# Kernel optimization log

Hardware: AMD Instinct MI355X
Metric: run time of the kernel (lower is better)

Reference implementation:

```python
import jax, jax.numpy as jnp
import numpy as np

N = 4096
CIN = 128
COUT = 128
J = 2
SLOPE = 0.2        # LeakyReLU negative slope (GAT-style)
NEG = -9.0e15      # mask fill value from the source
ATT = J * COUT     # att_slice


def _leaky(v):
    return jnp.where(v >= 0, v, SLOPE * v)


def setup_inputs() -> dict:
    key = jax.random.key(0)
    ks = jax.random.split(key, 12)
    x = jax.random.normal(ks[0], (N, CIN), dtype=jnp.float32)

    def sparse_op(k):
        kv, km = jax.random.split(k)
        vals = jax.random.normal(kv, (N, N), dtype=jnp.float32)
        mask = jax.random.uniform(km, (N, N)) < 0.05
        return jnp.where(mask, vals, 0.0)

    Lu = sparse_op(ks[1])
    Ld = sparse_op(ks[2])
    P = jax.random.normal(ks[3], (N, N), dtype=jnp.float32) * 0.01  # harmonic projector

    s = 1.0 / np.sqrt(CIN)
    Wi_w = jax.random.uniform(ks[4], (J, CIN, COUT), minval=-s, maxval=s)
    Wi_b = jax.random.uniform(ks[5], (J, COUT), minval=-s, maxval=s)
    Ws_w = jax.random.uniform(ks[6], (J, CIN, COUT), minval=-s, maxval=s)
    Ws_b = jax.random.uniform(ks[7], (J, COUT), minval=-s, maxval=s)
    Wh_w = jax.random.uniform(ks[8], (CIN, COUT), minval=-s, maxval=s)
    Wh_b = jax.random.uniform(ks[9], (COUT,), minval=-s, maxval=s)
    att_irr = jax.random.normal(ks[10], (2 * ATT, 1), dtype=jnp.float32) * 0.1
    att_sol = jax.random.normal(ks[11], (2 * ATT, 1), dtype=jnp.float32) * 0.1
    return {"x": x, "Lu": Lu, "Ld": Ld, "P": P,
            "Wi_w": Wi_w, "Wi_b": Wi_b, "Ws_w": Ws_w, "Ws_b": Ws_b,
            "Wh_w": Wh_w, "Wh_b": Wh_b, "att_irr": att_irr, "att_sol": att_sol}


def reference(x, Lu, Ld, P, Wi_w, Wi_b, Ws_w, Ws_b, Wh_w, Wh_b, att_irr, att_sol):
    n = x.shape[0]
    # concat_j W_irr[j](x) -> [N, J*COUT] (j-major matches torch.cat along dim=1)
    x_irr = (jnp.einsum('nc,jco->njo', x, Wi_w) + Wi_b[None]).reshape(n, ATT)
    x_sol = (jnp.einsum('nc,jco->njo', x, Ws_w) + Ws_b[None]).reshape(n, ATT)

    # GAT-style scores: E[i,j] = leaky(s1[i] + s2[j])
    E_irr = _leaky(x_irr @ att_irr[:ATT] + (x_irr @ att_irr[ATT:]).T)
    E_sol = _leaky(x_sol @ att_sol[:ATT] + (x_sol @ att_sol[ATT:]).T)
    E_irr = jnp.where(Ld != 0, E_irr, NEG)
    E_sol = jnp.where(Lu != 0, E_sol, NEG)
    alpha_irr = jax.nn.softmax(E_irr, axis=1)  # dropout: eval mode -> identity
    alpha_sol = jax.nn.softmax(E_sol, axis=1)

    z = (alpha_irr @ x) @ Wi_w[0] + Wi_b[0] + (alpha_sol @ x) @ Ws_w[0] + Ws_b[0]
    for p in range(1, J):  # Laplacian-power aggregation
        alpha_irr = alpha_irr @ Ld
        alpha_sol = alpha_sol @ Lu
        z = z + (alpha_irr @ x) @ Wi_w[p] + Wi_b[p]
        z = z + (alpha_sol @ x) @ Ws_w[p] + Ws_b[p]
    z = z + (P @ x) @ Wh_w + Wh_b
    return z
```

## Files before the change

kernel.cpp:

```cpp
#include <hip/hip_runtime.h>

#define NN 4096
#define SLOPE 0.2f

typedef float f4_t __attribute__((ext_vector_type(4)));
typedef __bf16 bf8v __attribute__((ext_vector_type(8)));
typedef float f32x16 __attribute__((ext_vector_type(16)));

#define V_OFF     0
#define C_OFF     512
#define BT_OFF    516
#define S_OFF     1024
#define HXI_OFF   32768
#define HXS_OFF   (HXI_OFF + NN*128)
#define UI_OFF    (HXS_OFF + NN*128)
#define US_OFF    (UI_OFF + NN*128)
#define XWH_OFF   (US_OFF + NN*128)
#define OI_OFF    (XWH_OFF + NN*128)
#define OS_OFF    (OI_OFF + NN*128)
#define ZP_OFF    (OS_OFF + NN*128)
#define WS_FLOATS (ZP_OFF + 8*NN*128)
#define XF_BYTE_OFF  ((size_t)WS_FLOATS * 4)
#define HX2_BYTE_OFF (XF_BYTE_OFF + (size_t)2*1024*1024)
#define DEN_BYTE_OFF (HX2_BYTE_OFF + (size_t)4*1024*1024)

#define XI(c)   ((c) + (((c) >> 5) << 2))

#define FRAG(c, k) ((size_t)((k) >> 4) * 2048 + (size_t)((c) >> 5) * 512 \
                    + (size_t)((((c) & 31) + 32 * (((k) >> 3) & 1)) * 8 + ((k) & 7)))

__device__ __forceinline__ unsigned short f2bf(float x) {
  unsigned u = __float_as_uint(x);
  return (unsigned short)((u + 0x7FFFu + ((u >> 16) & 1u)) >> 16);
}
__device__ __forceinline__ float bf2f(unsigned short h) {
  return __uint_as_float(((unsigned)h) << 16);
}
union BFU { unsigned short u[8]; bf8v v; };

__global__ __launch_bounds__(128) void k_prep(
    const float* __restrict__ Wi_w, const float* __restrict__ Wi_b,
    const float* __restrict__ Ws_w, const float* __restrict__ Ws_b,
    const float* __restrict__ Wh_b, const float* __restrict__ att_irr,
    const float* __restrict__ att_sol, float* __restrict__ ws) {
  const int t = threadIdx.x;
  float v1i = 0.f, v2i = 0.f, v1s = 0.f, v2s = 0.f;
  for (int j = 0; j < 2; ++j) {
    for (int o = 0; o < 128; ++o) {
      const float wi = Wi_w[j*16384 + t*128 + o];
      const float wv = Ws_w[j*16384 + t*128 + o];
      v1i += wi * att_irr[j*128 + o];
      v2i += wi * att_irr[256 + j*128 + o];
      v1s += wv * att_sol[j*128 + o];
      v2s += wv * att_sol[256 + j*128 + o];
    }
  }
  ws[V_OFF + t]       = v1i;
  ws[V_OFF + 128 + t] = v2i;
  ws[V_OFF + 256 + t] = v1s;
  ws[V_OFF + 384 + t] = v2s;
  ws[BT_OFF + t] = Wi_b[t] + Wi_b[128 + t] + Ws_b[t] + Ws_b[128 + t] + Wh_b[t];
  if (t < 4) {
    const float* bb = (t < 2) ? Wi_b : Ws_b;
    const float* aa = ((t < 2) ? att_irr : att_sol) + ((t & 1) ? 256 : 0);
    float c = 0.f;
    for (int k = 0; k < 256; ++k) c += bb[k] * aa[k];
    ws[C_OFF + t] = c;
  }
}

__global__ __launch_bounds__(256) void k_pre2(
    const float* __restrict__ x, const float* __restrict__ Wh_w,
    float* __restrict__ ws, unsigned short* __restrict__ xth,
    unsigned short* __restrict__ xtl, unsigned short* __restrict__ xfh,
    unsigned short* __restrict__ xfl) {
  __shared__ __align__(16) float At[32][33];
  __shared__ __align__(16) float Wt[32][144];
  const int t = threadIdx.x;

  if (blockIdx.x < 128) {
    const int rb = blockIdx.x;
    const int rg = t >> 4, cg = t & 15;
    const int r0 = rb * 32;
    float acc[2][8];
    #pragma unroll
    for (int i = 0; i < 2; ++i)
      #pragma unroll
      for (int j = 0; j < 8; ++j) acc[i][j] = 0.f;
    for (int k0 = 0; k0 < 128; k0 += 32) {
      __syncthreads();
      {
        const int row = t >> 3, kq = t & 7;
        const float4 av = *(const float4*)&x[(r0 + row)*128 + k0 + kq*4];
        At[row][kq*4+0] = av.x; At[row][kq*4+1] = av.y;
        At[row][kq*4+2] = av.z; At[row][kq*4+3] = av.w;
      }
      #pragma unroll
      for (int l = 0; l < 4; ++l) {
        const int idx = t + l*256;
        const int kr = idx >> 5, c4 = idx & 31;
        const float4 wv = *(const float4*)&Wh_w[(k0 + kr)*128 + c4*4];
        *(float4*)&Wt[kr][XI(c4*4)] = wv;
      }
      __syncthreads();
      #pragma unroll
      for (int k = 0; k < 32; ++k) {
        const float a0 = At[rg*2 + 0][k];
        const float a1 = At[rg*2 + 1][k];
        const float4 b0 = *(const float4*)&Wt[k][XI(cg*8)];
        const float4 b1 = *(const float4*)&Wt[k][XI(cg*8 + 4)];
        acc[0][0] += a0*b0.x; acc[0][1] += a0*b0.y; acc[0][2] += a0*b0.z; acc[0][3] += a0*b0.w;
        acc[0][4] += a0*b1.x; acc[0][5] += a0*b1.y; acc[0][6] += a0*b1.z; acc[0][7] += a0*b1.w;
        acc[1][0] += a1*b0.x; acc[1][1] += a1*b0.y; acc[1][2] += a1*b0.z; acc[1][3] += a1*b0.w;
        acc[1][4] += a1*b1.x; acc[1][5] += a1*b1.y; acc[1][6] += a1*b1.z; acc[1][7] += a1*b1.w;
      }
    }
    #pragma unroll
    for (int i = 0; i < 2; ++i) {
      const int r = r0 + rg*2 + i;
      #pragma unroll
      for (int j = 0; j < 8; ++j) {
        const int c = cg*8 + j;
        const float val = acc[i][j];
        const unsigned short h = f2bf(val);
        const unsigned short l = f2bf(val - bf2f(h));
        const size_t fa = FRAG(c, r);
        xth[fa] = h;
        xtl[fa] = l;
      }
    }
  } else {
    const int wave = t >> 6, lane = t & 63;
    const int row = (blockIdx.x - 128) * 4 + wave;
    const float* v = ws + V_OFF;
    const float x0 = x[row*128 + lane];
    const float x1 = x[row*128 + 64 + lane];
    {
      const unsigned short h0 = f2bf(x0);
      const unsigned short l0 = f2bf(x0 - bf2f(h0));
      const size_t fa0 = FRAG(lane, row);
      xfh[fa0] = h0; xfl[fa0] = l0;
      const unsigned short h1 = f2bf(x1);
      const unsigned short l1 = f2bf(x1 - bf2f(h1));
      const size_t fa1 = FRAG(lane + 64, row);
      xfh[fa1] = h1; xfl[fa1] = l1;
    }
    float p0 = x0 * v[lane]       + x1 * v[64 + lane];
    float p1 = x0 * v[128 + lane] + x1 * v[192 + lane];
    float p2 = x0 * v[256 + lane] + x1 * v[320 + lane];
    float p3 = x0 * v[384 + lane] + x1 * v[448 + lane];
    #pragma unroll
    for (int off = 32; off; off >>= 1) {
      p0 += __shfl_down(p0, off);
      p1 += __shfl_down(p1, off);
      p2 += __shfl_down(p2, off);
      p3 += __shfl_down(p3, off);
    }
    if (lane == 0) {
      ws[S_OFF + row]          = p0 + ws[C_OFF + 0];
      ws[S_OFF + NN + row]     = p1 + ws[C_OFF + 1];
      ws[S_OFF + 2*NN + row]   = p2 + ws[C_OFF + 2];
      ws[S_OFF + 3*NN + row]   = p3 + ws[C_OFF + 3];
    }
  }
}

__global__ __launch_bounds__(512) void k_hxmm(
    const float* __restrict__ Ld, const float* __restrict__ Lu,
    const unsigned short* __restrict__ xfh, const unsigned short* __restrict__ xfl,
    float* __restrict__ ws, float* __restrict__ hx2) {
  const int bid = blockIdx.x;
  const int br  = (bid >> 2) & 1;
  const int rest = ((bid >> 3) << 2) | (bid & 3);
  const int rblk = rest & 127;
  const int kz   = rest >> 7;
  const int t = threadIdx.x;
  const int lane = t & 63;
  const int n = (t >> 6) & 3, par = t >> 8;
  const int r0 = rblk * 32;
  const int kbase = kz * 2048;
  const float* __restrict__ L = br ? Lu : Ld;
  float* __restrict__ out = kz ? (hx2 + (size_t)br * NN * 128)
                               : (ws + (br ? HXS_OFF : HXI_OFF));

  __shared__ __align__(16) char ahb[2][8192];
  __shared__ __align__(16) char alb[2][8192];

  f32x16 acc;
  #pragma unroll
  for (int e = 0; e < 16; ++e) acc[e] = 0.f;

  const int srow = t >> 4;
  const int kg   = (t & 15) * 8;
  const int sS   = kg >> 4;
  const int lt   = srow + 32 * ((kg >> 3) & 1);
  const int soff = (sS * 64 + (lt ^ sS)) * 16;
  const float* __restrict__ lrow = L + (size_t)(r0 + srow) * NN + kbase + kg;

  const unsigned short* __restrict__ bh_w =
      xfh + ((size_t)(kbase >> 4) + par * 4) * 2048 + n * 512 + lane * 8;
  const unsigned short* __restrict__ bl_w =
      xfl + ((size_t)(kbase >> 4) + par * 4) * 2048 + n * 512 + lane * 8;

  bf8v bhA[4], blA[4], bhB[4], blB[4];

  f4_t va = *(const f4_t*)lrow;
  f4_t vb = *(const f4_t*)(lrow + 4);
  #pragma unroll
  for (int si = 0; si < 4; ++si) {
    bhA[si] = *(const bf8v*)(bh_w + (size_t)si * 2048);
    blA[si] = *(const bf8v*)(bl_w + (size_t)si * 2048);
  }
  {
    BFU ph, pl;
    #pragma unroll
    for (int c = 0; c < 8; ++c) {
      const float f = (c < 4) ? va[c] : vb[c - 4];
      const unsigned short hh = f2bf(f);
      ph.u[c] = hh;
      pl.u[c] = f2bf(f - bf2f(hh));
    }
    *(bf8v*)(ahb[0] + soff) = ph.v;
    *(bf8v*)(alb[0] + soff) = pl.v;
  }

  for (int m = 0; m < 8; ++m) {
    const int t1 = 2 * m + 1;
    f4_t na = *(const f4_t*)(lrow + t1 * 128);
    f4_t nb = *(const f4_t*)(lrow + t1 * 128 + 4);
    #pragma unroll
    for (int si = 0; si < 4; ++si) {
      bhB[si] = *(const bf8v*)(bh_w + ((size_t)t1 * 8 + si) * 2048);
      blB[si] = *(const bf8v*)(bl_w + ((size_t)t1 * 8 + si) * 2048);
    }
    __syncthreads();
    #pragma unroll
    for (int si = 0; si < 4; ++si) {
      const int s = par * 4 + si;
      const int ra16 = (s * 64 + (lane ^ s)) * 16;
      const bf8v ah = *(const bf8v*)(ahb[0] + ra16);
      const bf8v al = *(const bf8v*)(alb[0] + ra16);
      acc = __builtin_amdgcn_mfma_f32_32x32x16_bf16(ah, bhA[si], acc, 0, 0, 0);
      acc = __builtin_amdgcn_mfma_f32_32x32x16_bf16(al, bhA[si], acc, 0, 0, 0);
      acc = __builtin_amdgcn_mfma_f32_32x32x16_bf16(ah, blA[si], acc, 0, 0, 0);
    }
    {
      BFU ph, pl;
      #pragma unroll
      for (int c = 0; c < 8; ++c) {
        const float f = (c < 4) ? na[c] : nb[c - 4];
        const unsigned short hh = f2bf(f);
        ph.u[c] = hh;
        pl.u[c] = f2bf(f - bf2f(hh));
      }
      *(bf8v*)(ahb[1] + soff) = ph.v;
      *(bf8v*)(alb[1] + soff) = pl.v;
    }
    if (m < 7) {
      va = *(const f4_t*)(lrow + (t1 + 1) * 128);
      vb = *(const f4_t*)(lrow + (t1 + 1) * 128 + 4);
      #pragma unroll
      for (int si = 0; si < 4; ++si) {
        bhA[si] = *(const bf8v*)(bh_w + ((size_t)(t1 + 1) * 8 + si) * 2048);
        blA[si] = *(const bf8v*)(bl_w + ((size_t)(t1 + 1) * 8 + si) * 2048);
      }
    }
    __syncthreads();
    #pragma unroll
    for (int si = 0; si < 4; ++si) {
      const int s = par * 4 + si;
      const int ra16 = (s * 64 + (lane ^ s)) * 16;
      const bf8v ah = *(const bf8v*)(ahb[1] + ra16);
      const bf8v al = *(const bf8v*)(alb[1] + ra16);
      acc = __builtin_amdgcn_mfma_f32_32x32x16_bf16(ah, bhB[si], acc, 0, 0, 0);
      acc = __builtin_amdgcn_mfma_f32_32x32x16_bf16(al, bhB[si], acc, 0, 0, 0);
      acc = __builtin_amdgcn_mfma_f32_32x32x16_bf16(ah, blB[si], acc, 0, 0, 0);
    }
    if (m < 7) {
      BFU ph, pl;
      #pragma unroll
      for (int c = 0; c < 8; ++c) {
        const float f = (c < 4) ? va[c] : vb[c - 4];
        const unsigned short hh = f2bf(f);
        ph.u[c] = hh;
        pl.u[c] = f2bf(f - bf2f(hh));
      }
      *(bf8v*)(ahb[0] + soff) = ph.v;
      *(bf8v*)(alb[0] + soff) = pl.v;
    }
  }

  float* red = (float*)&ahb[0][0];
  __syncthreads();
  const int la = lane & 31;
  if (par == 1) {
    #pragma unroll
    for (int reg = 0; reg < 16; ++reg) {
      const int row = (reg & 3) + 8*(reg >> 2) + 4*(lane >> 5);
      red[n*1024 + row*32 + la] = acc[reg];
    }
  }
  __syncthreads();
  if (par == 0) {
    #pragma unroll
    for (int reg = 0; reg < 16; ++reg) {
      const int row = (reg & 3) + 8*(reg >> 2) + 4*(lane >> 5);
      out[(size_t)(r0 + row) * 128 + n*32 + la] = acc[reg] + red[n*1024 + row*32 + la];
    }
  }
}

__global__ __launch_bounds__(256) void k_ugemm(
    const float* __restrict__ x, const float* __restrict__ Wi_w,
    const float* __restrict__ Ws_w, float* __restrict__ ws,
    const float* __restrict__ hx2,
    unsigned short* __restrict__ uih, unsigned short* __restrict__ uil,
    unsigned short* __restrict__ ush, unsigned short* __restrict__ usl) {
  const int rb = blockIdx.x;
  const int sel = blockIdx.y;
  const float* A[2]; const float* A2[2]; const float* W[2];
  unsigned short* uh; unsigned short* ul;
  if (sel == 0) { A[0]=x; A2[0]=nullptr; W[0]=Wi_w;
                  A[1]=ws+HXI_OFF; A2[1]=hx2; W[1]=Wi_w+16384; uh=uih; ul=uil; }
  else          { A[0]=x; A2[0]=nullptr; W[0]=Ws_w;
                  A[1]=ws+HXS_OFF; A2[1]=hx2+(size_t)NN*128; W[1]=Ws_w+16384; uh=ush; ul=usl; }

  __shared__ __align__(16) float At[32][33];
  __shared__ __align__(16) float Wt[32][144];
  const int t = threadIdx.x;
  const int rg = t >> 4, cg = t & 15;
  const int r0 = rb * 32;
  float acc[2][8];
  #pragma unroll
  for (int i = 0; i < 2; ++i)
    #pragma unroll
    for (int j = 0; j < 8; ++j) acc[i][j] = 0.f;

  for (int ps = 0; ps < 2; ++ps) {
    const float* __restrict__ Ap = A[ps];
    const float* __restrict__ Ap2 = A2[ps];
    const float* __restrict__ Wp = W[ps];
    for (int k0 = 0; k0 < 128; k0 += 32) {
      __syncthreads();
      {
        const int row = t >> 3, kq = t & 7;
        float4 av = *(const float4*)&Ap[(r0 + row)*128 + k0 + kq*4];
        if (Ap2) {
          const float4 av2 = *(const float4*)&Ap2[(r0 + row)*128 + k0 + kq*4];
          av.x += av2.x; av.y += av2.y; av.z += av2.z; av.w += av2.w;
        }
        At[row][kq*4+0] = av.x; At[row][kq*4+1] = av.y;
        At[row][kq*4+2] = av.z; At[row][kq*4+3] = av.w;
      }
      #pragma unroll
      for (int l = 0; l < 4; ++l) {
        const int idx = t + l*256;
        const int kr = idx >> 5, c4 = idx & 31;
        const float4 wv = *(const float4*)&Wp[(k0 + kr)*128 + c4*4];
        *(float4*)&Wt[kr][XI(c4*4)] = wv;
      }
      __syncthreads();
      #pragma unroll
      for (int k = 0; k < 32; ++k) {
        const float a0 = At[rg*2 + 0][k];
        const float a1 = At[rg*2 + 1][k];
        const float4 b0 = *(const float4*)&Wt[k][XI(cg*8)];
        const float4 b1 = *(const float4*)&Wt[k][XI(cg*8 + 4)];
        acc[0][0] += a0*b0.x; acc[0][1] += a0*b0.y; acc[0][2] += a0*b0.z; acc[0][3] += a0*b0.w;
        acc[0][4] += a0*b1.x; acc[0][5] += a0*b1.y; acc[0][6] += a0*b1.z; acc[0][7] += a0*b1.w;
        acc[1][0] += a1*b0.x; acc[1][1] += a1*b0.y; acc[1][2] += a1*b0.z; acc[1][3] += a1*b0.w;
        acc[1][4] += a1*b1.x; acc[1][5] += a1*b1.y; acc[1][6] += a1*b1.z; acc[1][7] += a1*b1.w;
      }
    }
  }
  #pragma unroll
  for (int i = 0; i < 2; ++i) {
    const int r = r0 + rg*2 + i;
    #pragma unroll
    for (int j = 0; j < 8; ++j) {
      const int c = cg*8 + j;
      const float val = acc[i][j];
      const unsigned short h = f2bf(val);
      const unsigned short l = f2bf(val - bf2f(h));
      const size_t fa = FRAG(c, r);
      uh[fa] = h;
      ul[fa] = l;
    }
  }
}

__global__ __launch_bounds__(512) void k_attnmm(
    const float* __restrict__ Ld, const float* __restrict__ Lu,
    float* __restrict__ ws, const unsigned short* __restrict__ uih,
    const unsigned short* __restrict__ uil, const unsigned short* __restrict__ ush,
    const unsigned short* __restrict__ usl, float* __restrict__ denp) {
  const int bid = blockIdx.x;
  const int br  = (bid >> 2) & 1;
  const int rest = ((bid >> 3) << 2) | (bid & 3);
  const int rblk = rest & 127;
  const int kz   = rest >> 7;
  const int t = threadIdx.x;
  const int lane = t & 63;
  const int n = (t >> 6) & 3, par = t >> 8;
  const int r0 = rblk * 32;
  const int kbase = kz * 2048;
  const float* __restrict__ L = br ? Lu : Ld;
  const unsigned short* __restrict__ ufh = br ? ush : uih;
  const unsigned short* __restrict__ ufl = br ? usl : uil;
  float* __restrict__ out = kz ? (ws + (br ? HXS_OFF : HXI_OFF))
                               : (ws + (br ? OS_OFF : OI_OFF));
  float* __restrict__ dout = denp + (size_t)(kz * 2 + br) * NN;
  const float* __restrict__ s1b = ws + S_OFF + (br ? 2*NN : 0) + r0;
  const float* __restrict__ s2b = ws + S_OFF + (br ? 3*NN : NN) + kbase;

  __shared__ __align__(16) char ahb[2][8192];
  __shared__ __align__(16) char alb[2][8192];
  __shared__ float dend[32][16];

  f32x16 acc;
  #pragma unroll
  for (int e = 0; e < 16; ++e) acc[e] = 0.f;
  float dp = 0.f;

  const int srow = t >> 4;
  const int kg   = (t & 15) * 8;
  const int sS   = kg >> 4;
  const int lt   = srow + 32 * ((kg >> 3) & 1);
  const int soff = (sS * 64 + (lt ^ sS)) * 16;
  const float s1v = s1b[srow];
  const float* __restrict__ lrow = L + (size_t)(r0 + srow) * NN + kbase + kg;
  const float* __restrict__ s2r  = s2b + kg;

  const unsigned short* __restrict__ bh_w =
      ufh + ((size_t)(kbase >> 4) + par * 4) * 2048 + n * 512 + lane * 8;
  const unsigned short* __restrict__ bl_w =
      ufl + ((size_t)(kbase >> 4) + par * 4) * 2048 + n * 512 + lane * 8;

  bf8v bhA[4], blA[4], bhB[4], blB[4];

  f4_t va = *(const f4_t*)lrow;
  f4_t vb = *(const f4_t*)(lrow + 4);
  f4_t sa = *(const f4_t*)s2r;
  f4_t sb = *(const f4_t*)(s2r + 4);
  #pragma unroll
  for (int si = 0; si < 4; ++si) {
    bhA[si] = *(const bf8v*)(bh_w + (size_t)si * 2048);
    blA[si] = *(const bf8v*)(bl_w + (size_t)si * 2048);
  }
  {
    BFU ph, pl;
    #pragma unroll
    for (int c = 0; c < 8; ++c) {
      const float Lv = (c < 4) ? va[c] : vb[c - 4];
      const float s2 = (c < 4) ? sa[c] : sb[c - 4];
      const float sc = s1v + s2;
      const float scl = sc >= 0.f ? sc : SLOPE * sc;
      const float ex = (Lv != 0.f) ? __expf(scl) : 0.f;
      dp += ex;
      const unsigned short hh = f2bf(ex);
      ph.u[c] = hh;
      pl.u[c] = f2bf(ex - bf2f(hh));
    }
    *(bf8v*)(ahb[0] + soff) = ph.v;
    *(bf8v*)(alb[0] + soff) = pl.v;
  }

  for (int m = 0; m < 8; ++m) {
    const int t1 = 2 * m + 1;
    f4_t na = *(const f4_t*)(lrow + t1 * 128);
    f4_t nb = *(const f4_t*)(lrow + t1 * 128 + 4);
    f4_t nsa = *(const f4_t*)(s2r + t1 * 128);
    f4_t nsb = *(const f4_t*)(s2r + t1 * 128 + 4);
    #pragma unroll
    for (int si = 0; si < 4; ++si) {
      bhB[si] = *(const bf8v*)(bh_w + ((size_t)t1 * 8 + si) * 2048);
      blB[si] = *(const bf8v*)(bl_w + ((size_t)t1 * 8 + si) * 2048);
    }
    __syncthreads();
    #pragma unroll
    for (int si = 0; si < 4; ++si) {
      const int s = par * 4 + si;
      const int ra16 = (s * 64 + (lane ^ s)) * 16;
      const bf8v ah = *(const bf8v*)(ahb[0] + ra16);
      const bf8v al = *(const bf8v*)(alb[0] + ra16);
      acc = __builtin_amdgcn_mfma_f32_32x32x16_bf16(ah, bhA[si], acc, 0, 0, 0);
      acc = __builtin_amdgcn_mfma_f32_32x32x16_bf16(al, bhA[si], acc, 0, 0, 0);
      acc = __builtin_amdgcn_mfma_f32_32x32x16_bf16(ah, blA[si], acc, 0, 0, 0);
    }
    {
      BFU ph, pl;
      #pragma unroll
      for (int c = 0; c < 8; ++c) {
        const float Lv = (c < 4) ? na[c] : nb[c - 4];
        const float s2 = (c < 4) ? nsa[c] : nsb[c - 4];
        const float sc = s1v + s2;
        const float scl = sc >= 0.f ? sc : SLOPE * sc;
        const float ex = (Lv != 0.f) ? __expf(scl) : 0.f;
        dp += ex;
        const unsigned short hh = f2bf(ex);
        ph.u[c] = hh;
        pl.u[c] = f2bf(ex - bf2f(hh));
      }
      *(bf8v*)(ahb[1] + soff) = ph.v;
      *(bf8v*)(alb[1] + soff) = pl.v;
    }
    if (m < 7) {
      va = *(const f4_t*)(lrow + (t1 + 1) * 128);
      vb = *(const f4_t*)(lrow + (t1 + 1) * 128 + 4);
      sa = *(const f4_t*)(s2r + (t1 + 1) * 128);
      sb = *(const f4_t*)(s2r + (t1 + 1) * 128 + 4);
      #pragma unroll
      for (int si = 0; si < 4; ++si) {
        bhA[si] = *(const bf8v*)(bh_w + ((size_t)(t1 + 1) * 8 + si) * 2048);
        blA[si] = *(const bf8v*)(bl_w + ((size_t)(t1 + 1) * 8 + si) * 2048);
      }
    }
    __syncthreads();
    #pragma unroll
    for (int si = 0; si < 4; ++si) {
      const int s = par * 4 + si;
      const int ra16 = (s * 64 + (lane ^ s)) * 16;
      const bf8v ah = *(const bf8v*)(ahb[1] + ra16);
      const bf8v al = *(const bf8v*)(alb[1] + ra16);
      acc = __builtin_amdgcn_mfma_f32_32x32x16_bf16(ah, bhB[si], acc, 0, 0, 0);
      acc = __builtin_amdgcn_mfma_f32_32x32x16_bf16(al, bhB[si], acc, 0, 0, 0);
      acc = __builtin_amdgcn_mfma_f32_32x32x16_bf16(ah, blB[si], acc, 0, 0, 0);
    }
    if (m < 7) {
      BFU ph, pl;
      #pragma unroll
      for (int c = 0; c < 8; ++c) {
        const float Lv = (c < 4) ? va[c] : vb[c - 4];
        const float s2 = (c < 4) ? sa[c] : sb[c - 4];
        const float sc = s1v + s2;
        const float scl = sc >= 0.f ? sc : SLOPE * sc;
        const float ex = (Lv != 0.f) ? __expf(scl) : 0.f;
        dp += ex;
        const unsigned short hh = f2bf(ex);
        ph.u[c] = hh;
        pl.u[c] = f2bf(ex - bf2f(hh));
      }
      *(bf8v*)(ahb[0] + soff) = ph.v;
      *(bf8v*)(alb[0] + soff) = pl.v;
    }
  }

  dend[srow][t & 15] = dp;
  float* red = (float*)&ahb[0][0];
  __syncthreads();
  if (t < 32) {
    float d = 0.f;
    #pragma unroll
    for (int i = 0; i < 16; ++i) d += dend[t][i];
    dout[r0 + t] = d;
  }
  const int la = lane & 31;
  if (par == 1) {
    #pragma unroll
    for (int reg = 0; reg < 16; ++reg) {
      const int row = (reg & 3) + 8*(reg >> 2) + 4*(lane >> 5);
      red[n*1024 + row*32 + la] = acc[reg];
    }
  }
  __syncthreads();
  if (par == 0) {
    #pragma unroll
    for (int reg = 0; reg < 16; ++reg) {
      const int row = (reg & 3) + 8*(reg >> 2) + 4*(lane >> 5);
      out[(size_t)(r0 + row) * 128 + n*32 + la] = acc[reg] + red[n*1024 + row*32 + la];
    }
  }
}

__global__ __launch_bounds__(256) void k_pgemm(
    const float* __restrict__ P, const unsigned short* __restrict__ xth,
    const unsigned short* __restrict__ xtl, float* __restrict__ zpart) {
  const int t = threadIdx.x;
  const int w = t >> 6, lane = t & 63;
  const int la = lane & 31;
  const int koff = (lane >> 5) * 8;
  const int r0 = blockIdx.x * 32;
  const int kz = blockIdx.y;
  const int kb = kz * 512 + w * 128;

  f32x16 acc[4];
  #pragma unroll
  for (int n = 0; n < 4; ++n)
    #pragma unroll
    for (int e = 0; e < 16; ++e) acc[n][e] = 0.f;

  const float* __restrict__ arow = P + (size_t)(r0 + la) * NN + kb + koff;
  const unsigned short* __restrict__ bh_base = xth + (size_t)kb * 128 + lane * 8;
  const unsigned short* __restrict__ bl_base = xtl + (size_t)kb * 128 + lane * 8;

  f4_t a0 = __builtin_nontemporal_load((const f4_t*)arow);
  f4_t a1 = __builtin_nontemporal_load((const f4_t*)(arow + 4));
  for (int s = 0; s < 8; ++s) {
    f4_t na0 = a0, na1 = a1;
    if (s < 7) {
      na0 = __builtin_nontemporal_load((const f4_t*)(arow + (s + 1) * 16));
      na1 = __builtin_nontemporal_load((const f4_t*)(arow + (s + 1) * 16 + 4));
    }
    BFU ah, al;
    #pragma unroll
    for (int i = 0; i < 8; ++i) {
      const float f = (i < 4) ? a0[i] : a1[i - 4];
      const unsigned short h = f2bf(f);
      ah.u[i] = h;
      al.u[i] = f2bf(f - bf2f(h));
    }
    const unsigned short* __restrict__ bh_s = bh_base + s * 2048;
    const unsigned short* __restrict__ bl_s = bl_base + s * 2048;
    #pragma unroll
    for (int n = 0; n < 4; ++n) {
      const bf8v bh = *(const bf8v*)(bh_s + n * 512);
      const bf8v bl = *(const bf8v*)(bl_s + n * 512);
      acc[n] = __builtin_amdgcn_mfma_f32_32x32x16_bf16(ah.v, bh, acc[n], 0, 0, 0);
      acc[n] = __builtin_amdgcn_mfma_f32_32x32x16_bf16(al.v, bh, acc[n], 0, 0, 0);
      acc[n] = __builtin_amdgcn_mfma_f32_32x32x16_bf16(ah.v, bl, acc[n], 0, 0, 0);
    }
    a0 = na0; a1 = na1;
  }

  __shared__ float red[2][32][128];
  if (w < 2) {
    #pragma unroll
    for (int n = 0; n < 4; ++n)
      #pragma unroll
      for (int reg = 0; reg < 16; ++reg) {
        const int row = (reg & 3) + 8*(reg >> 2) + 4*(lane >> 5);
        red[w][row][32*n + la] = acc[n][reg];
      }
  }
  __syncthreads();
  if (w >= 2) {
    #pragma unroll
    for (int n = 0; n < 4; ++n)
      #pragma unroll
      for (int reg = 0; reg < 16; ++reg) {
        const int row = (reg & 3) + 8*(reg >> 2) + 4*(lane >> 5);
        red[w - 2][row][32*n + la] += acc[n][reg];
      }
  }
  __syncthreads();
  float* __restrict__ zp = zpart + (size_t)kz * NN * 128;
  #pragma unroll
  for (int i = 0; i < 8; ++i) {
    const int row = w * 8 + i;
    zp[(size_t)(r0 + row) * 128 + lane]      = red[0][row][lane]      + red[1][row][lane];
    zp[(size_t)(r0 + row) * 128 + 64 + lane] = red[0][row][64 + lane] + red[1][row][64 + lane];
  }
}

__global__ __launch_bounds__(256) void k_combine(const float* __restrict__ ws,
                                                 const float* __restrict__ denp,
                                                 float* __restrict__ z) {
  const int i = blockIdx.x * 256 + threadIdx.x;
  const int col = i & 127;
  const int row = i >> 7;
  const float di = denp[row] + denp[2*NN + row];
  const float ds = denp[NN + row] + denp[3*NN + row];
  const float oi = ws[OI_OFF + i] + ws[HXI_OFF + i];
  const float os = ws[OS_OFF + i] + ws[HXS_OFF + i];
  float acc = ws[BT_OFF + col] + oi / di + os / ds;
  #pragma unroll
  for (int kz = 0; kz < 8; ++kz) acc += ws[ZP_OFF + kz*NN*128 + i];
  z[i] = acc;
}

extern "C" void kernel_launch(void* const* d_in, const int* in_sizes, int n_in,
                              void* d_out, int out_size, void* d_ws, size_t ws_size,
                              hipStream_t stream) {
  const float* x       = (const float*)d_in[0];
  const float* Lu      = (const float*)d_in[1];
  const float* Ld      = (const float*)d_in[2];
  const float* P       = (const float*)d_in[3];
  const float* Wi_w    = (const float*)d_in[4];
  const float* Wi_b    = (const float*)d_in[5];
  const float* Ws_w    = (const float*)d_in[6];
  const float* Ws_b    = (const float*)d_in[7];
  const float* Wh_w    = (const float*)d_in[8];
  const float* Wh_b    = (const float*)d_in[9];
  const float* att_irr = (const float*)d_in[10];
  const float* att_sol = (const float*)d_in[11];
  float* z  = (float*)d_out;
  float* ws = (float*)d_ws;
  float*          zpart = ws + ZP_OFF;
  unsigned short* xth   = (unsigned short*)(ws + XWH_OFF);
  unsigned short* xtl   = xth + (size_t)128 * NN;
  unsigned short* uih   = (unsigned short*)(ws + UI_OFF);
  unsigned short* uil   = uih + (size_t)128 * NN;
  unsigned short* ush   = (unsigned short*)(ws + US_OFF);
  unsigned short* usl   = ush + (size_t)128 * NN;
  unsigned short* xfh   = (unsigned short*)((char*)d_ws + XF_BYTE_OFF);
  unsigned short* xfl   = xfh + (size_t)128 * NN;
  float*          hx2   = (float*)((char*)d_ws + HX2_BYTE_OFF);
  float*          denp  = (float*)((char*)d_ws + DEN_BYTE_OFF);

  k_prep<<<1, 128, 0, stream>>>(Wi_w, Wi_b, Ws_w, Ws_b, Wh_b, att_irr, att_sol, ws);
  k_pre2<<<1152, 256, 0, stream>>>(x, Wh_w, ws, xth, xtl, xfh, xfl);
  k_hxmm<<<512, 512, 0, stream>>>(Ld, Lu, xfh, xfl, ws, hx2);
  {
    dim3 g(128, 2);
    k_ugemm<<<g, 256, 0, stream>>>(x, Wi_w, Ws_w, ws, hx2, uih, uil, ush, usl);
  }
  k_attnmm<<<512, 512, 0, stream>>>(Ld, Lu, ws, uih, uil, ush, usl, denp);
  {
    dim3 g(128, 8);
    k_pgemm<<<g, 256, 0, stream>>>(P, xth, xtl, zpart);
  }
  k_combine<<<NN * 128 / 256, 256, 0, stream>>>(ws, denp, z);
}
```

Baseline: 360.9 us.

## Cache nonzero bitmask of Ld/Lu in hxmm and reuse in attention matmul

While streaming Ld/Lu in k_hxmm, each thread packs a nonzero bitmask byte for its 8 elements and writes it to workspace. k_attnmm then reads this bitmask (1 bit per element) instead of re-reading the full fp32 Ld/Lu matrices (2×64MB), cutting global memory traffic in the attention kernel. The mask buffer reuses the zpart region, which k_pgemm overwrites only after k_attnmm has run. The cost is extra byte-sized scattered stores in k_hxmm.

```diff
diff --git a/kernel.cpp b/kernel.cpp
--- a/kernel.cpp
+++ b/kernel.cpp
@@ -168,7 +168,8 @@
 __global__ __launch_bounds__(512) void k_hxmm(
     const float* __restrict__ Ld, const float* __restrict__ Lu,
     const unsigned short* __restrict__ xfh, const unsigned short* __restrict__ xfl,
-    float* __restrict__ ws, float* __restrict__ hx2) {
+    float* __restrict__ ws, float* __restrict__ hx2,
+    unsigned char* __restrict__ msk) {
   const int bid = blockIdx.x;
   const int br  = (bid >> 2) & 1;
   const int rest = ((bid >> 3) << 2) | (bid & 3);
@@ -196,6 +197,8 @@
   const int lt   = srow + 32 * ((kg >> 3) & 1);
   const int soff = (sS * 64 + (lt ^ sS)) * 16;
   const float* __restrict__ lrow = L + (size_t)(r0 + srow) * NN + kbase + kg;
+  unsigned char* __restrict__ mwr =
+      msk + (size_t)br * NN * 512 + (size_t)(r0 + srow) * 512 + (kbase >> 3) + (t & 15);
 
   const unsigned short* __restrict__ bh_w =
       xfh + ((size_t)(kbase >> 4) + par * 4) * 2048 + n * 512 + lane * 8;
@@ -212,16 +215,18 @@
     blA[si] = *(const bf8v*)(bl_w + (size_t)si * 2048);
   }
   {
-    BFU ph, pl;
+    BFU ph, pl; unsigned mb = 0;
     #pragma unroll
     for (int c = 0; c < 8; ++c) {
       const float f = (c < 4) ? va[c] : vb[c - 4];
+      mb |= (f != 0.f) ? (1u << c) : 0u;
       const unsigned short hh = f2bf(f);
       ph.u[c] = hh;
       pl.u[c] = f2bf(f - bf2f(hh));
     }
     *(bf8v*)(ahb[0] + soff) = ph.v;
     *(bf8v*)(alb[0] + soff) = pl.v;
+    mwr[0] = (unsigned char)mb;
   }
 
   for (int m = 0; m < 8; ++m) {
@@ -245,16 +250,18 @@
       acc = __builtin_amdgcn_mfma_f32_32x32x16_bf16(ah, blA[si], acc, 0, 0, 0);
     }
     {
-      BFU ph, pl;
+      BFU ph, pl; unsigned mb = 0;
       #pragma unroll
       for (int c = 0; c < 8; ++c) {
         const float f = (c < 4) ? na[c] : nb[c - 4];
+        mb |= (f != 0.f) ? (1u << c) : 0u;
         const unsigned short hh = f2bf(f);
         ph.u[c] = hh;
         pl.u[c] = f2bf(f - bf2f(hh));
       }
       *(bf8v*)(ahb[1] + soff) = ph.v;
       *(bf8v*)(alb[1] + soff) = pl.v;
+      mwr[t1 * 16] = (unsigned char)mb;
     }
     if (m < 7) {
       va = *(const f4_t*)(lrow + (t1 + 1) * 128);
@@ -277,16 +284,18 @@
       acc = __builtin_amdgcn_mfma_f32_32x32x16_bf16(ah, blB[si], acc, 0, 0, 0);
     }
     if (m < 7) {
-      BFU ph, pl;
+      BFU ph, pl; unsigned mb = 0;
       #pragma unroll
       for (int c = 0; c < 8; ++c) {
         const float f = (c < 4) ? va[c] : vb[c - 4];
+        mb |= (f != 0.f) ? (1u << c) : 0u;
         const unsigned short hh = f2bf(f);
         ph.u[c] = hh;
         pl.u[c] = f2bf(f - bf2f(hh));
       }
       *(bf8v*)(ahb[0] + soff) = ph.v;
       *(bf8v*)(alb[0] + soff) = pl.v;
+      mwr[(t1 + 1) * 16] = (unsigned char)mb;
     }
   }
 
@@ -390,10 +399,10 @@
 }
 
 __global__ __launch_bounds__(512) void k_attnmm(
-    const float* __restrict__ Ld, const float* __restrict__ Lu,
     float* __restrict__ ws, const unsigned short* __restrict__ uih,
     const unsigned short* __restrict__ uil, const unsigned short* __restrict__ ush,
-    const unsigned short* __restrict__ usl, float* __restrict__ denp) {
+    const unsigned short* __restrict__ usl, float* __restrict__ denp,
+    const unsigned char* __restrict__ msk) {
   const int bid = blockIdx.x;
   const int br  = (bid >> 2) & 1;
   const int rest = ((bid >> 3) << 2) | (bid & 3);
@@ -404,7 +413,6 @@
   const int n = (t >> 6) & 3, par = t >> 8;
   const int r0 = rblk * 32;
   const int kbase = kz * 2048;
-  const float* __restrict__ L = br ? Lu : Ld;
   const unsigned short* __restrict__ ufh = br ? ush : uih;
   const unsigned short* __restrict__ ufl = br ? usl : uil;
   float* __restrict__ out = kz ? (ws + (br ? HXS_OFF : HXI_OFF))
@@ -428,8 +436,9 @@
   const int lt   = srow + 32 * ((kg >> 3) & 1);
   const int soff = (sS * 64 + (lt ^ sS)) * 16;
   const float s1v = s1b[srow];
-  const float* __restrict__ lrow = L + (size_t)(r0 + srow) * NN + kbase + kg;
-  const float* __restrict__ s2r  = s2b + kg;
+  const unsigned char* __restrict__ mrd =
+      msk + (size_t)br * NN * 512 + (size_t)(r0 + srow) * 512 + (kbase >> 3) + (t & 15);
+  const float* __restrict__ s2r = s2b + kg;
 
   const unsigned short* __restrict__ bh_w =
       ufh + ((size_t)(kbase >> 4) + par * 4) * 2048 + n * 512 + lane * 8;
@@ -438,8 +447,7 @@
 
   bf8v bhA[4], blA[4], bhB[4], blB[4];
 
-  f4_t va = *(const f4_t*)lrow;
-  f4_t vb = *(const f4_t*)(lrow + 4);
+  unsigned mka = mrd[0];
   f4_t sa = *(const f4_t*)s2r;
   f4_t sb = *(const f4_t*)(s2r + 4);
   #pragma unroll
@@ -451,11 +459,10 @@
     BFU ph, pl;
     #pragma unroll
     for (int c = 0; c < 8; ++c) {
-      const float Lv = (c < 4) ? va[c] : vb[c - 4];
       const float s2 = (c < 4) ? sa[c] : sb[c - 4];
       const float sc = s1v + s2;
       const float scl = sc >= 0.f ? sc : SLOPE * sc;
-      const float ex = (Lv != 0.f) ? __expf(scl) : 0.f;
+      const float ex = ((mka >> c) & 1u) ? __expf(scl) : 0.f;
       dp += ex;
       const unsigned short hh = f2bf(ex);
       ph.u[c] = hh;
@@ -467,8 +474,7 @@
 
   for (int m = 0; m < 8; ++m) {
     const int t1 = 2 * m + 1;
-    f4_t na = *(const f4_t*)(lrow + t1 * 128);
-    f4_t nb = *(const f4_t*)(lrow + t1 * 128 + 4);
+    unsigned mkb = mrd[t1 * 16];
     f4_t nsa = *(const f4_t*)(s2r + t1 * 128);
     f4_t nsb = *(const f4_t*)(s2r + t1 * 128 + 4);
     #pragma unroll
@@ -491,11 +497,10 @@
       BFU ph, pl;
       #pragma unroll
       for (int c = 0; c < 8; ++c) {
-        const float Lv = (c < 4) ? na[c] : nb[c - 4];
         const float s2 = (c < 4) ? nsa[c] : nsb[c - 4];
         const float sc = s1v + s2;
         const float scl = sc >= 0.f ? sc : SLOPE * sc;
-        const float ex = (Lv != 0.f) ? __expf(scl) : 0.f;
+        const float ex = ((mkb >> c) & 1u) ? __expf(scl) : 0.f;
         dp += ex;
         const unsigned short hh = f2bf(ex);
         ph.u[c] = hh;
@@ -505,8 +510,7 @@
       *(bf8v*)(alb[1] + soff) = pl.v;
     }
     if (m < 7) {
-      va = *(const f4_t*)(lrow + (t1 + 1) * 128);
-      vb = *(const f4_t*)(lrow + (t1 + 1) * 128 + 4);
+      mka = mrd[(t1 + 1) * 16];
       sa = *(const f4_t*)(s2r + (t1 + 1) * 128);
       sb = *(const f4_t*)(s2r + (t1 + 1) * 128 + 4);
       #pragma unroll
@@ -530,11 +534,10 @@
       BFU ph, pl;
       #pragma unroll
       for (int c = 0; c < 8; ++c) {
-        const float Lv = (c < 4) ? va[c] : vb[c - 4];
         const float s2 = (c < 4) ? sa[c] : sb[c - 4];
         const float sc = s1v + s2;
         const float scl = sc >= 0.f ? sc : SLOPE * sc;
-        const float ex = (Lv != 0.f) ? __expf(scl) : 0.f;
+        const float ex = ((mka >> c) & 1u) ? __expf(scl) : 0.f;
         dp += ex;
         const unsigned short hh = f2bf(ex);
         ph.u[c] = hh;
@@ -686,6 +689,7 @@
   float* z  = (float*)d_out;
   float* ws = (float*)d_ws;
   float*          zpart = ws + ZP_OFF;
+  unsigned char*  msk   = (unsigned char*)(ws + ZP_OFF);
   unsigned short* xth   = (unsigned short*)(ws + XWH_OFF);
   unsigned short* xtl   = xth + (size_t)128 * NN;
   unsigned short* uih   = (unsigned short*)(ws + UI_OFF);
@@ -699,12 +703,12 @@
 
   k_prep<<<1, 128, 0, stream>>>(Wi_w, Wi_b, Ws_w, Ws_b, Wh_b, att_irr, att_sol, ws);
   k_pre2<<<1152, 256, 0, stream>>>(x, Wh_w, ws, xth, xtl, xfh, xfl);
-  k_hxmm<<<512, 512, 0, stream>>>(Ld, Lu, xfh, xfl, ws, hx2);
+  k_hxmm<<<512, 512, 0, stream>>>(Ld, Lu, xfh, xfl, ws, hx2, msk);
   {
     dim3 g(128, 2);
     k_ugemm<<<g, 256, 0, stream>>>(x, Wi_w, Ws_w, ws, hx2, uih, uil, ush, usl);
   }
-  k_attnmm<<<512, 512, 0, stream>>>(Ld, Lu, ws, uih, uil, ush, usl, denp);
+  k_attnmm<<<512, 512, 0, stream>>>(ws, uih, uil, ush, usl, denp, msk);
   {
     dim3 g(128, 8);
     k_pgemm<<<g, 256, 0, stream>>>(P, xth, xtl, zpart);
```

Result: no change. 365.4 us (+1.2%).
